# Optimization experiments

Hardware: AMD Instinct MI355X
Metric: run time of the kernel (lower is better)

The kernel has to match this reference:

```python
import jax, jax.numpy as jnp
import numpy as np

B, Lq, C, NH, NP, DFF = 8, 10000, 256, 8, 4, 1024
H_IMG, W_IMG = 100, 100
HD = C // NH


def _layer_norm(x, g, b, eps=1e-5):
    m = jnp.mean(x, -1, keepdims=True)
    v = jnp.mean((x - m) ** 2, -1, keepdims=True)
    return (x - m) / jnp.sqrt(v + eps) * g + b


def _bilinear_sample(value, loc, Hs, Ws):
    # value: [B, Lin, NH, HD]; loc: [B, Lq, NH, NP, 2] normalized to [0,1]
    vt = jnp.transpose(value, (0, 2, 1, 3))  # [B, NH, Lin, HD]
    # move to [B, NH, Lq, NP] layout once; grid_sample(align_corners=False) pixel coords
    x = jnp.transpose(loc[..., 0], (0, 2, 1, 3)) * Ws - 0.5
    y = jnp.transpose(loc[..., 1], (0, 2, 1, 3)) * Hs - 0.5
    x0 = jnp.floor(x); y0 = jnp.floor(y)
    lx = x - x0; ly = y - y0

    def corner(xi, yi, w):
        valid = (xi >= 0) & (xi < Ws) & (yi >= 0) & (yi < Hs)
        xc = jnp.clip(xi, 0, Ws - 1).astype(jnp.int32)
        yc = jnp.clip(yi, 0, Hs - 1).astype(jnp.int32)
        idx = (yc * Ws + xc).reshape(B, NH, Lq * NP, 1)
        v = jnp.take_along_axis(vt, idx, axis=2).reshape(B, NH, Lq, NP, HD)
        return v * (w * valid)[..., None]

    acc = corner(x0, y0, (1 - lx) * (1 - ly))
    acc = acc + corner(x0 + 1, y0, lx * (1 - ly))
    acc = acc + corner(x0, y0 + 1, (1 - lx) * ly)
    acc = acc + corner(x0 + 1, y0 + 1, lx * ly)
    return acc  # [B, NH, Lq, NP, HD]


def setup_inputs() -> dict:
    key = jax.random.key(0)
    ks = jax.random.split(key, 12)
    s = 0.02
    return {
        "query": jax.random.normal(ks[0], (B, Lq, C), jnp.float32),
        "src": jax.random.normal(ks[1], (B, H_IMG * W_IMG, C), jnp.float32),
        "reference_points": jax.random.uniform(ks[2], (B, Lq, 1, 2), jnp.float32),
        "spatial_shapes": jnp.array([[H_IMG, W_IMG]], dtype=jnp.int64),
        "level_start_index": jnp.array([0], dtype=jnp.int64),
        "W_off": jax.random.normal(ks[3], (C, NH * NP * 2), jnp.float32) * s,
        "b_off": jnp.zeros((NH * NP * 2,), jnp.float32),
        "W_aw": jax.random.normal(ks[4], (C, NH * NP), jnp.float32) * s,
        "b_aw": jnp.zeros((NH * NP,), jnp.float32),
        "W_val": jax.random.normal(ks[5], (C, C), jnp.float32) * s,
        "b_val": jnp.zeros((C,), jnp.float32),
        "W_out": jax.random.normal(ks[6], (C, C), jnp.float32) * s,
        "b_out": jnp.zeros((C,), jnp.float32),
        "g1": jnp.ones((C,), jnp.float32),
        "be1": jnp.zeros((C,), jnp.float32),
        "W1": jax.random.normal(ks[7], (C, DFF), jnp.float32) * s,
        "b1": jnp.zeros((DFF,), jnp.float32),
        "W2": jax.random.normal(ks[8], (DFF, C), jnp.float32) * s,
        "b2": jnp.zeros((C,), jnp.float32),
        "g2": jnp.ones((C,), jnp.float32),
        "be2": jnp.zeros((C,), jnp.float32),
    }


def reference(query, src, reference_points, spatial_shapes, level_start_index,
              W_off, b_off, W_aw, b_aw, W_val, b_val, W_out, b_out,
              g1, be1, W1, b1, W2, b2, g2, be2):
    Hs = spatial_shapes[0, 0]
    Ws = spatial_shapes[0, 1]
    # MSDeformAttn (n_levels = 1)
    value = (src @ W_val + b_val).reshape(B, -1, NH, HD)
    off = (query @ W_off + b_off).reshape(B, Lq, NH, NP, 2)
    aw = jax.nn.softmax((query @ W_aw + b_aw).reshape(B, Lq, NH, NP), axis=-1)
    normalizer = jnp.stack([Ws, Hs]).astype(query.dtype)  # (W, H)
    loc = reference_points[:, :, None] + off / normalizer  # [B,Lq,NH,NP,2]
    sampled = _bilinear_sample(value, loc, Hs, Ws)  # [B,NH,Lq,NP,HD]
    attn = jnp.einsum('bhqpd,bqhp->bqhd', sampled, aw).reshape(B, Lq, C)
    attn = attn @ W_out + b_out
    # residual + LN + FFN + LN
    q = _layer_norm(query + attn, g1, be1)
    ffn = jax.nn.relu(q @ W1 + b1) @ W2 + b2
    return _layer_norm(q + ffn, g2, be2)
```

## Files before the change

kernel.cpp:

```cpp
#include <hip/hip_runtime.h>
#include <hip/hip_bf16.h>

typedef __hip_bfloat16 bf16;
typedef unsigned short u16;
typedef short short8 __attribute__((ext_vector_type(8)));
typedef float f32x4 __attribute__((ext_vector_type(4)));

static constexpr int B_   = 8;
static constexpr int Lq_  = 10000;
static constexpr int C_   = 256;
static constexpr int NH_  = 8;
static constexpr int NP_  = 4;
static constexpr int HIMG = 100;
static constexpr int WIMG = 100;
static constexpr int LIN  = 10000;

__device__ __forceinline__ u16 f2bf(float x) {
    union { bf16 b; u16 u; } cv; cv.b = __float2bfloat16(x); return cv.u;
}
__device__ __forceinline__ float bf2f(u16 u) {
    return __uint_as_float((unsigned)u << 16);
}

__device__ __forceinline__ void gl_lds16(const void* g, void* l) {
    __builtin_amdgcn_global_load_lds(
        (const __attribute__((address_space(1))) void*)g,
        (__attribute__((address_space(3))) void*)l, 16, 0, 0);
}
__device__ __forceinline__ void drain_barrier() {
    asm volatile("s_waitcnt vmcnt(0) lgkmcnt(0)" ::: "memory");
    __builtin_amdgcn_s_barrier();
}

template <int AMODE, int EPI>
__global__ __launch_bounds__(512, 2) void gemm256(
    const void* __restrict__ Av, const u16* __restrict__ Bg,
    const float* __restrict__ bias, const void* __restrict__ resid,
    const float* __restrict__ gw, const float* __restrict__ bw,
    void* __restrict__ Cv, int K, int ldc)
{
    __shared__ __align__(16) u16 At[2][128 * 64];
    __shared__ __align__(16) u16 Bt[2][256 * 64];
    __shared__ float red[2][128][4];

    const int tid  = threadIdx.x;
    const int lane = tid & 63;
    const int w    = tid >> 6;
    const int wm   = w >> 2, wn = w & 3;
    const int m0   = blockIdx.x * 128;
    const int n0   = blockIdx.y * 256;
    const u16* BgB = Bg + (size_t)n0 * K;

    f32x4 acc[4][4];
#pragma unroll
    for (int i = 0; i < 4; ++i)
#pragma unroll
        for (int j = 0; j < 4; ++j) acc[i][j] = f32x4{0.f, 0.f, 0.f, 0.f};

    auto stageA = [&](int t) {
        const int kt = t << 6;
        if constexpr (AMODE == 0) {
            const int row = tid >> 2;
            const int k0  = (tid & 3) << 4;
            const float* s = (const float*)Av + (size_t)(m0 + row) * K + kt + k0;
            float4 v0 = *(const float4*)(s + 0);
            float4 v1 = *(const float4*)(s + 4);
            float4 v2 = *(const float4*)(s + 8);
            float4 v3 = *(const float4*)(s + 12);
            union { short8 s8; u16 u[8]; } ga, gb;
            ga.u[0]=f2bf(v0.x); ga.u[1]=f2bf(v0.y); ga.u[2]=f2bf(v0.z); ga.u[3]=f2bf(v0.w);
            ga.u[4]=f2bf(v1.x); ga.u[5]=f2bf(v1.y); ga.u[6]=f2bf(v1.z); ga.u[7]=f2bf(v1.w);
            gb.u[0]=f2bf(v2.x); gb.u[1]=f2bf(v2.y); gb.u[2]=f2bf(v2.z); gb.u[3]=f2bf(v2.w);
            gb.u[4]=f2bf(v3.x); gb.u[5]=f2bf(v3.y); gb.u[6]=f2bf(v3.z); gb.u[7]=f2bf(v3.w);
            u16* d = &At[t & 1][row * 64];
            *(short8*)&d[(k0)     ^ ((row & 7) << 3)] = ga.s8;
            *(short8*)&d[(k0 + 8) ^ ((row & 7) << 3)] = gb.s8;
        } else if constexpr (AMODE == 1) {
#pragma unroll
            for (int i = 0; i < 2; ++i) {
                const int rb  = w * 16 + i * 8;
                const int row = rb + (lane >> 3);
                const int gs  = (lane & 7) ^ (row & 7);
                gl_lds16((const u16*)Av + (size_t)(m0 + row) * K + kt + gs * 8,
                         &At[t & 1][rb * 64]);
            }
        } else {
#pragma unroll
            for (int i = 0; i < 2; ++i) {
                const int rb  = w * 16 + i * 8;
                const int row = rb + (lane >> 3);
                gl_lds16((const u16*)Av + (size_t)(m0 + row) * K + kt + (lane & 7) * 8,
                         &At[t & 1][rb * 64]);
            }
        }
    };
    auto stageB = [&](int t) {
        const int kt = t << 6;
#pragma unroll
        for (int i = 0; i < 4; ++i) {
            const int rb  = w * 32 + i * 8;
            const int row = rb + (lane >> 3);
            gl_lds16(BgB + (size_t)row * K + kt + (lane & 7) * 8,
                     &Bt[t & 1][rb * 64]);
        }
    };
    auto compute = [&](int t) {
        const u16* a = At[t & 1];
        const u16* b = Bt[t & 1];
#pragma unroll
        for (int ks = 0; ks < 2; ++ks) {
            const int ko = ks * 32 + ((lane >> 4) << 3);
            short8 bfr[4];
#pragma unroll
            for (int n = 0; n < 4; ++n) {
                const int nr = wn * 64 + n * 16 + (lane & 15);
                bfr[n] = *(const short8*)&b[nr * 64 + (ko ^ ((nr & 7) << 3))];
            }
#pragma unroll
            for (int m = 0; m < 4; ++m) {
                const int ar = wm * 64 + m * 16 + (lane & 15);
                const short8 af = *(const short8*)&a[ar * 64 + (ko ^ ((ar & 7) << 3))];
#pragma unroll
                for (int n = 0; n < 4; ++n)
                    acc[m][n] = __builtin_amdgcn_mfma_f32_16x16x32_bf16(
                        af, bfr[n], acc[m][n], 0, 0, 0);
            }
        }
    };

    stageA(0); stageB(0);
    drain_barrier();
    const int nt = K >> 6;
    for (int t = 0; t < nt; ++t) {
        if (t + 1 < nt) { stageA(t + 1); stageB(t + 1); }
        compute(t);
        drain_barrier();
    }

    float bcol[4], gcol[4], becol[4];
#pragma unroll
    for (int n = 0; n < 4; ++n) {
        const int col = wn * 64 + n * 16 + (lane & 15);
        bcol[n] = bias[n0 + col];
        if (EPI >= 2) { gcol[n] = gw[col]; becol[n] = bw[col]; }
    }

    if constexpr (EPI <= 1) {
        u16* Co = (u16*)Cv;
#pragma unroll
        for (int m = 0; m < 4; ++m)
#pragma unroll
            for (int r = 0; r < 4; ++r) {
                const int lr = wm * 64 + m * 16 + (lane >> 4) * 4 + r;
#pragma unroll
                for (int n = 0; n < 4; ++n) {
                    const int col = wn * 64 + n * 16 + (lane & 15);
                    float v = acc[m][n][r] + bcol[n];
                    if (EPI == 1) v = fmaxf(v, 0.f);
                    Co[(size_t)(m0 + lr) * ldc + n0 + col] = f2bf(v);
                }
            }
    } else {
        float s[4][4], s2[4][4];
#pragma unroll
        for (int m = 0; m < 4; ++m)
#pragma unroll
            for (int r = 0; r < 4; ++r) {
                const int lr = wm * 64 + m * 16 + (lane >> 4) * 4 + r;
                float ps = 0.f, ps2 = 0.f;
#pragma unroll
                for (int n = 0; n < 4; ++n) {
                    const int col = wn * 64 + n * 16 + (lane & 15);
                    float rv;
                    if constexpr (EPI == 2)
                        rv = ((const float*)resid)[(size_t)(m0 + lr) * 256 + col];
                    else
                        rv = bf2f(((const u16*)resid)[(size_t)(m0 + lr) * 256
                                                      + (col ^ ((lr & 7) << 3))]);
                    float v = acc[m][n][r] + bcol[n] + rv;
                    acc[m][n][r] = v;
                    ps += v; ps2 += v * v;
                }
#pragma unroll
                for (int o = 1; o < 16; o <<= 1) {
                    ps  += __shfl_xor(ps,  o);
                    ps2 += __shfl_xor(ps2, o);
                }
                s[m][r] = ps; s2[m][r] = ps2;
            }
        if ((lane & 15) == 0) {
#pragma unroll
            for (int m = 0; m < 4; ++m)
#pragma unroll
                for (int r = 0; r < 4; ++r) {
                    const int lr = wm * 64 + m * 16 + (lane >> 4) * 4 + r;
                    red[0][lr][wn] = s[m][r];
                    red[1][lr][wn] = s2[m][r];
                }
        }
        __syncthreads();
        if (tid < 128) {
            const float ss  = red[0][tid][0] + red[0][tid][1] + red[0][tid][2] + red[0][tid][3];
            const float ss2 = red[1][tid][0] + red[1][tid][1] + red[1][tid][2] + red[1][tid][3];
            const float mean = ss * (1.f / 256.f);
            const float var  = fmaxf(ss2 * (1.f / 256.f) - mean * mean, 0.f);
            red[0][tid][0] = mean;
            red[1][tid][0] = rsqrtf(var + 1e-5f);
        }
        __syncthreads();
#pragma unroll
        for (int m = 0; m < 4; ++m)
#pragma unroll
            for (int r = 0; r < 4; ++r) {
                const int lr = wm * 64 + m * 16 + (lane >> 4) * 4 + r;
                const float mean = red[0][lr][0];
                const float rstd = red[1][lr][0];
#pragma unroll
                for (int n = 0; n < 4; ++n) {
                    const int col = wn * 64 + n * 16 + (lane & 15);
                    const float o = (acc[m][n][r] - mean) * rstd * gcol[n] + becol[n];
                    if constexpr (EPI == 2)
                        ((u16*)Cv)[(size_t)(m0 + lr) * 256 + (col ^ ((lr & 7) << 3))] = f2bf(o);
                    else
                        ((float*)Cv)[(size_t)(m0 + lr) * 256 + col] = o;
                }
            }
    }
}

__global__ __launch_bounds__(256) void gemm_oaw(
    const float* __restrict__ Av, const u16* __restrict__ Bt,
    const float* __restrict__ bias, float* __restrict__ C,
    int M, int K, int Nreal, int ldc)
{
    __shared__ __align__(16) u16 Asl[2][128 * 32];
    __shared__ __align__(16) u16 Bsl[2][128 * 32];

    const int tid  = threadIdx.x;
    const int lane = tid & 63;
    const int w    = tid >> 6;
    const int wr   = (w >> 1) * 64;
    const int wc   = (w & 1) * 64;
    const int m0   = blockIdx.y * 128;
    const int n0   = blockIdx.x * 128;

    const int srow = lane >> 2;
    const int scol = (lane & 3) << 3;
    const u16* bG = Bt + (size_t)(n0 + w * 32 + srow) * K + scol;
    const size_t rstep16 = (size_t)16 * K;

    const int ar  = lane >> 3;
    const int ac  = (lane & 7) << 2;
    const float* aGf = Av + (size_t)(m0 + w * 32 + ar) * K + ac;

    const int aRoff = (wr + (lane & 15)) * 32 + (lane >> 4) * 8;
    const int bRoff = (wc + (lane & 15)) * 32 + (lane >> 4) * 8;

    f32x4 acc[4][4];
#pragma unroll
    for (int i = 0; i < 4; ++i)
#pragma unroll
        for (int j = 0; j < 4; ++j) acc[i][j] = f32x4{0.f, 0.f, 0.f, 0.f};

    float4 a4[4];
    const int nt = K >> 5;

#pragma unroll
    for (int rep = 0; rep < 4; ++rep)
        a4[rep] = *(const float4*)(aGf + (size_t)(rep * 8) * K);
#pragma unroll
    for (int rep = 0; rep < 4; ++rep) {
        ushort4 v{f2bf(a4[rep].x), f2bf(a4[rep].y), f2bf(a4[rep].z), f2bf(a4[rep].w)};
        *(ushort4*)&Asl[0][(w * 32 + rep * 8 + ar) * 32 + ac] = v;
    }
    gl_lds16(bG, &Bsl[0][(w * 32) * 32]);
    gl_lds16(bG + rstep16, &Bsl[0][(w * 32 + 16) * 32]);
    drain_barrier();

    for (int t = 0; t < nt; ++t) {
        const int cur = t & 1, nxt = cur ^ 1;
        const int k0n = (t + 1) << 5;
        const bool has_next = (t + 1 < nt);
        if (has_next) {
#pragma unroll
            for (int rep = 0; rep < 4; ++rep)
                a4[rep] = *(const float4*)(aGf + k0n + (size_t)(rep * 8) * K);
            gl_lds16(bG + k0n, &Bsl[nxt][(w * 32) * 32]);
            gl_lds16(bG + k0n + rstep16, &Bsl[nxt][(w * 32 + 16) * 32]);
        }
        short8 af[4], bfr[4];
#pragma unroll
        for (int m = 0; m < 4; ++m) af[m]  = *(const short8*)&Asl[cur][aRoff + m * 16 * 32];
#pragma unroll
        for (int n = 0; n < 4; ++n) bfr[n] = *(const short8*)&Bsl[cur][bRoff + n * 16 * 32];
#pragma unroll
        for (int m = 0; m < 4; ++m)
#pragma unroll
            for (int n = 0; n < 4; ++n)
                acc[m][n] = __builtin_amdgcn_mfma_f32_16x16x32_bf16(
                    af[m], bfr[n], acc[m][n], 0, 0, 0);
        if (has_next) {
#pragma unroll
            for (int rep = 0; rep < 4; ++rep) {
                ushort4 v{f2bf(a4[rep].x), f2bf(a4[rep].y), f2bf(a4[rep].z), f2bf(a4[rep].w)};
                *(ushort4*)&Asl[nxt][(w * 32 + rep * 8 + ar) * 32 + ac] = v;
            }
        }
        drain_barrier();
    }

#pragma unroll
    for (int n = 0; n < 4; ++n) {
        const int gc = n0 + wc + n * 16 + (lane & 15);
        if (gc >= Nreal) continue;
        const float bv = bias[gc];
        const int gr0 = m0 + wr + (lane >> 4) * 4;
#pragma unroll
        for (int m = 0; m < 4; ++m)
#pragma unroll
            for (int r = 0; r < 4; ++r)
                C[(size_t)(gr0 + m * 16 + r) * ldc + gc] = acc[m][n][r] + bv;
    }
}

__global__ __launch_bounds__(256) void prep_all(
    const float* __restrict__ Wv, const float* __restrict__ Wo,
    const float* __restrict__ W1, const float* __restrict__ W2,
    const float* __restrict__ Woff, const float* __restrict__ Waw,
    const float* __restrict__ boff, const float* __restrict__ baw,
    u16* __restrict__ Wvs, u16* __restrict__ Wos,
    u16* __restrict__ W1g, u16* __restrict__ W2g,
    u16* __restrict__ Woa, float* __restrict__ boa)
{
    const int idx = blockIdx.x * 256 + threadIdx.x;
    if (idx < 65536) {
        const int n = idx >> 8, kd = idx & 255;
        const int k = (kd & ~63) | ((kd & 63) ^ ((n & 7) << 3));
        Wvs[idx] = f2bf(Wv[(size_t)k * 256 + n]);
    } else if (idx < 131072) {
        const int i = idx - 65536, n = i >> 8, kd = i & 255;
        const int k = (kd & ~63) | ((kd & 63) ^ ((n & 7) << 3));
        Wos[i] = f2bf(Wo[(size_t)k * 256 + n]);
    } else if (idx < 393216) {
        const int i = idx - 131072, n = i >> 8, kd = i & 255;
        const int k = (kd & ~63) | ((kd & 63) ^ ((n & 7) << 3));
        W1g[i] = f2bf(W1[(size_t)k * 1024 + n]);
    } else if (idx < 655360) {
        const int i = idx - 393216, n = i >> 10, kd = i & 1023;
        const int k = (kd & ~63) | ((kd & 63) ^ ((n & 7) << 3));
        W2g[i] = f2bf(W2[(size_t)k * 256 + n]);
    } else if (idx < 688128) {
        const int i = idx - 655360, n = i >> 8, k = i & 255;
        float v = 0.f;
        if (n < 64)      v = Woff[(size_t)k * 64 + n];
        else if (n < 96) v = Waw[(size_t)k * 32 + (n - 64)];
        Woa[i] = f2bf(v);
    } else if (idx < 688256) {
        const int i = idx - 688128;
        boa[i] = (i < 64) ? boff[i] : (i < 96 ? baw[i - 64] : 0.f);
    }
}

__global__ __launch_bounds__(256) void sample_attn(
    const u16* __restrict__ val, const float* __restrict__ oaw,
    const float* __restrict__ refp, u16* __restrict__ attn)
{
    const int t   = threadIdx.x;
    const int gid = blockIdx.x * 64 + (t >> 2);
    const int c0  = (t & 3) << 3;
    const int h   = gid & (NH_ - 1);
    const int bq  = gid >> 3;

    const float* row = oaw + (size_t)bq * 96;
    const float rx = refp[(size_t)bq * 2 + 0] * (float)WIMG;
    const float ry = refp[(size_t)bq * 2 + 1] * (float)HIMG;

    const float4 aw4 = *(const float4*)(row + 64 + h * 4);
    const float mx = fmaxf(fmaxf(aw4.x, aw4.y), fmaxf(aw4.z, aw4.w));
    const float e0 = __expf(aw4.x - mx), e1 = __expf(aw4.y - mx);
    const float e2 = __expf(aw4.z - mx), e3 = __expf(aw4.w - mx);
    const float inv = 1.f / (e0 + e1 + e2 + e3);
    const float w4[4] = {e0 * inv, e1 * inv, e2 * inv, e3 * inv};

    const int b = bq / Lq_;
    const u16* vb = val + (size_t)b * LIN * C_ + h * 32 + c0;

    float acc[8] = {};
#pragma unroll
    for (int p = 0; p < NP_; ++p) {
        const float2 off = *(const float2*)(row + (h * 4 + p) * 2);
        const float x = rx + off.x - 0.5f;
        const float y = ry + off.y - 0.5f;
        const float xf = floorf(x), yf = floorf(y);
        const float lx = x - xf, ly = y - yf;
        const int x0 = (int)xf, y0 = (int)yf;
        const float wp = w4[p];
        const float w00 = wp * (1.f - lx) * (1.f - ly);
        const float w10 = wp * lx * (1.f - ly);
        const float w01 = wp * (1.f - lx) * ly;
        const float w11 = wp * lx * ly;

#pragma unroll
        for (int c = 0; c < 4; ++c) {
            const int xi = x0 + (c & 1);
            const int yi = y0 + (c >> 1);
            const float wc = (c == 0) ? w00 : (c == 1) ? w10 : (c == 2) ? w01 : w11;
            const bool v = ((unsigned)xi < (unsigned)WIMG) & ((unsigned)yi < (unsigned)HIMG);
            const int idx = v ? (yi * WIMG + xi) : 0;
            const float w = v ? wc : 0.f;
            const short8 d = *(const short8*)(vb + (size_t)idx * C_);
#pragma unroll
            for (int j = 0; j < 8; ++j)
                acc[j] = fmaf(w, bf2f(((const u16*)&d)[j]), acc[j]);
        }
    }

    union { short8 s; u16 u[8]; } o;
#pragma unroll
    for (int j = 0; j < 8; ++j) o.u[j] = f2bf(acc[j]);
    *(short8*)(attn + (size_t)bq * C_ + h * 32 + c0) = o.s;
}

extern "C" void kernel_launch(void* const* d_in, const int* in_sizes, int n_in,
                              void* d_out, int out_size, void* d_ws, size_t ws_size,
                              hipStream_t stream)
{
    const float* query = (const float*)d_in[0];
    const float* src   = (const float*)d_in[1];
    const float* refp  = (const float*)d_in[2];
    const float* W_off = (const float*)d_in[5];
    const float* b_off = (const float*)d_in[6];
    const float* W_aw  = (const float*)d_in[7];
    const float* b_aw  = (const float*)d_in[8];
    const float* W_val = (const float*)d_in[9];
    const float* b_val = (const float*)d_in[10];
    const float* W_out = (const float*)d_in[11];
    const float* b_out = (const float*)d_in[12];
    const float* g1    = (const float*)d_in[13];
    const float* be1   = (const float*)d_in[14];
    const float* W1    = (const float*)d_in[15];
    const float* b1    = (const float*)d_in[16];
    const float* W2    = (const float*)d_in[17];
    const float* b2    = (const float*)d_in[18];
    const float* g2    = (const float*)d_in[19];
    const float* be2   = (const float*)d_in[20];
    float* out = (float*)d_out;

    char* ws = (char*)d_ws;

    u16*  val  = (u16*)(ws + 0);
    float* oaw = (float*)(ws + 40960000);
    u16*  attn = (u16*)(ws + 71680000);
    u16*  q1b  = (u16*)(ws + 112640000);
    u16*  h    = (u16*)(ws + 153600000);
    u16*  Wvs  = (u16*)(ws + 317440000);
    u16*  Wos  = (u16*)(ws + 317440000 + 131072);
    u16*  W1g  = (u16*)(ws + 317440000 + 262144);
    u16*  W2g  = (u16*)(ws + 317440000 + 786432);
    u16*  Woa  = (u16*)(ws + 317440000 + 1310720);
    float* boa = (float*)(ws + 317440000 + 1376256);

    prep_all<<<2689, 256, 0, stream>>>(W_val, W_out, W1, W2, W_off, W_aw,
                                       b_off, b_aw, Wvs, Wos, W1g, W2g,
                                       Woa, boa);

    gemm256<0, 0><<<dim3(625, 1), 512, 0, stream>>>(
        src, Wvs, b_val, nullptr, nullptr, nullptr, val, 256, 256);

    gemm_oaw<<<dim3(1, 625), 256, 0, stream>>>(
        query, Woa, boa, oaw, B_ * Lq_, 256, 96, 96);

    sample_attn<<<10000, 256, 0, stream>>>(val, oaw, refp, attn);

    gemm256<1, 2><<<dim3(625, 1), 512, 0, stream>>>(
        attn, Wos, b_out, query, g1, be1, q1b, 256, 256);

    gemm256<2, 1><<<dim3(625, 4), 512, 0, stream>>>(
        q1b, W1g, b1, nullptr, nullptr, nullptr, h, 256, 1024);

    gemm256<1, 3><<<dim3(625, 1), 512, 0, stream>>>(
        h, W2g, b2, q1b, g2, be2, out, 1024, 256);
}
```

Baseline: 360.4 us.

## Fuse FFN up and down GEMMs into one kernel keeping hidden activations on-chip

Replaces the separate W1 GEMM (writing a bf16 hidden tensor to global memory) and the W2 GEMM with LayerNorm epilogue by a single ffn_wave kernel. Each wave holds its 16-row strip of q1 in registers and loops over 128-wide hidden chunks, staging pre-swizzled W1/W2 tiles into LDS with double buffering. ReLU'd hidden chunks go through a per-wave LDS scratch and are immediately multiplied by W2 into register accumulators. This removes the large h write/read round trip and one launch, at the cost of heavy register pressure (many accumulators plus A fragments) and re-streaming all weights per block.

```diff
diff --git a/kernel.cpp b/kernel.cpp
--- a/kernel.cpp
+++ b/kernel.cpp
@@ -32,12 +32,12 @@
     __builtin_amdgcn_s_barrier();
 }
 
-template <int AMODE, int EPI>
+template <bool AF32, bool LN>
 __global__ __launch_bounds__(512, 2) void gemm256(
     const void* __restrict__ Av, const u16* __restrict__ Bg,
-    const float* __restrict__ bias, const void* __restrict__ resid,
+    const float* __restrict__ bias, const float* __restrict__ resid,
     const float* __restrict__ gw, const float* __restrict__ bw,
-    void* __restrict__ Cv, int K, int ldc)
+    u16* __restrict__ Co, int K)
 {
     __shared__ __align__(16) u16 At[2][128 * 64];
     __shared__ __align__(16) u16 Bt[2][256 * 64];
@@ -48,8 +48,6 @@
     const int w    = tid >> 6;
     const int wm   = w >> 2, wn = w & 3;
     const int m0   = blockIdx.x * 128;
-    const int n0   = blockIdx.y * 256;
-    const u16* BgB = Bg + (size_t)n0 * K;
 
     f32x4 acc[4][4];
 #pragma unroll
@@ -59,7 +57,7 @@
 
     auto stageA = [&](int t) {
         const int kt = t << 6;
-        if constexpr (AMODE == 0) {
+        if constexpr (AF32) {
             const int row = tid >> 2;
             const int k0  = (tid & 3) << 4;
             const float* s = (const float*)Av + (size_t)(m0 + row) * K + kt + k0;
@@ -75,7 +73,7 @@
             u16* d = &At[t & 1][row * 64];
             *(short8*)&d[(k0)     ^ ((row & 7) << 3)] = ga.s8;
             *(short8*)&d[(k0 + 8) ^ ((row & 7) << 3)] = gb.s8;
-        } else if constexpr (AMODE == 1) {
+        } else {
 #pragma unroll
             for (int i = 0; i < 2; ++i) {
                 const int rb  = w * 16 + i * 8;
@@ -84,14 +82,6 @@
                 gl_lds16((const u16*)Av + (size_t)(m0 + row) * K + kt + gs * 8,
                          &At[t & 1][rb * 64]);
             }
-        } else {
-#pragma unroll
-            for (int i = 0; i < 2; ++i) {
-                const int rb  = w * 16 + i * 8;
-                const int row = rb + (lane >> 3);
-                gl_lds16((const u16*)Av + (size_t)(m0 + row) * K + kt + (lane & 7) * 8,
-                         &At[t & 1][rb * 64]);
-            }
         }
     };
     auto stageB = [&](int t) {
@@ -100,7 +90,7 @@
         for (int i = 0; i < 4; ++i) {
             const int rb  = w * 32 + i * 8;
             const int row = rb + (lane >> 3);
-            gl_lds16(BgB + (size_t)row * K + kt + (lane & 7) * 8,
+            gl_lds16(Bg + (size_t)row * K + kt + (lane & 7) * 8,
                      &Bt[t & 1][rb * 64]);
         }
     };
@@ -141,12 +131,11 @@
 #pragma unroll
     for (int n = 0; n < 4; ++n) {
         const int col = wn * 64 + n * 16 + (lane & 15);
-        bcol[n] = bias[n0 + col];
-        if (EPI >= 2) { gcol[n] = gw[col]; becol[n] = bw[col]; }
-    }
-
-    if constexpr (EPI <= 1) {
-        u16* Co = (u16*)Cv;
+        bcol[n] = bias[col];
+        if (LN) { gcol[n] = gw[col]; becol[n] = bw[col]; }
+    }
+
+    if constexpr (!LN) {
 #pragma unroll
         for (int m = 0; m < 4; ++m)
 #pragma unroll
@@ -155,9 +144,7 @@
 #pragma unroll
                 for (int n = 0; n < 4; ++n) {
                     const int col = wn * 64 + n * 16 + (lane & 15);
-                    float v = acc[m][n][r] + bcol[n];
-                    if (EPI == 1) v = fmaxf(v, 0.f);
-                    Co[(size_t)(m0 + lr) * ldc + n0 + col] = f2bf(v);
+                    Co[(size_t)(m0 + lr) * 256 + col] = f2bf(acc[m][n][r] + bcol[n]);
                 }
             }
     } else {
@@ -171,13 +158,8 @@
 #pragma unroll
                 for (int n = 0; n < 4; ++n) {
                     const int col = wn * 64 + n * 16 + (lane & 15);
-                    float rv;
-                    if constexpr (EPI == 2)
-                        rv = ((const float*)resid)[(size_t)(m0 + lr) * 256 + col];
-                    else
-                        rv = bf2f(((const u16*)resid)[(size_t)(m0 + lr) * 256
-                                                      + (col ^ ((lr & 7) << 3))]);
-                    float v = acc[m][n][r] + bcol[n] + rv;
+                    float v = acc[m][n][r] + bcol[n]
+                            + resid[(size_t)(m0 + lr) * 256 + col];
                     acc[m][n][r] = v;
                     ps += v; ps2 += v * v;
                 }
@@ -219,12 +201,153 @@
                 for (int n = 0; n < 4; ++n) {
                     const int col = wn * 64 + n * 16 + (lane & 15);
                     const float o = (acc[m][n][r] - mean) * rstd * gcol[n] + becol[n];
-                    if constexpr (EPI == 2)
-                        ((u16*)Cv)[(size_t)(m0 + lr) * 256 + (col ^ ((lr & 7) << 3))] = f2bf(o);
-                    else
-                        ((float*)Cv)[(size_t)(m0 + lr) * 256 + col] = o;
+                    Co[(size_t)(m0 + lr) * 256 + col] = f2bf(o);
                 }
             }
+    }
+}
+
+__global__ __launch_bounds__(512, 2) void ffn_wave(
+    const u16* __restrict__ q1l, const u16* __restrict__ W1L,
+    const u16* __restrict__ W2L, const float* __restrict__ b1,
+    const float* __restrict__ b2, const float* __restrict__ g2w,
+    const float* __restrict__ be2, float* __restrict__ out)
+{
+    __shared__ __align__(16) u16 R0[16384];
+    __shared__ __align__(16) u16 R1[16384];
+    __shared__ __align__(16) u16 Hsc[8][2048];
+
+    const int tid  = threadIdx.x;
+    const int lane = tid & 63;
+    const int w    = tid >> 6;
+    const int m0   = blockIdx.x * 128;
+    const int strip = w * 16;
+    const int l15  = lane & 15;
+    const int lq   = lane >> 4;
+
+    short8 af[8];
+    {
+        const u16* aG = q1l + (size_t)(m0 + strip + l15) * 256 + lq * 8;
+#pragma unroll
+        for (int t = 0; t < 8; ++t)
+            af[t] = *(const short8*)(aG + t * 32);
+    }
+
+    auto stage = [&](const u16* src, u16* dst) {
+#pragma unroll
+        for (int i = 0; i < 4; ++i)
+            gl_lds16(src + (w * 4 + i) * 512 + lane * 8,
+                     dst + (w * 4 + i) * 512);
+    };
+
+    f32x4 acc2[16];
+#pragma unroll
+    for (int i = 0; i < 16; ++i) acc2[i] = f32x4{0.f, 0.f, 0.f, 0.f};
+
+    f32x4 acc1[8];
+    auto g1half = [&](const u16* Rg, int half) {
+#pragma unroll
+        for (int tl = 0; tl < 4; ++tl) {
+            const int t = half * 4 + tl;
+#pragma unroll
+            for (int nf = 0; nf < 8; ++nf) {
+                const int n = nf * 16 + l15;
+                const short8 bfr = *(const short8*)
+                    &Rg[n * 128 + (((tl * 4 + lq) ^ (n & 7)) << 3)];
+                acc1[nf] = __builtin_amdgcn_mfma_f32_16x16x32_bf16(
+                    af[t], bfr, acc1[nf], 0, 0, 0);
+            }
+        }
+    };
+    auto g2half = [&](const u16* Rg, int hu) {
+#pragma unroll
+        for (int ul = 0; ul < 2; ++ul) {
+            const int u = hu * 2 + ul;
+            const short8 hf = *(const short8*)
+                &Hsc[w][l15 * 128 + (((u * 4 + lq) ^ (l15 & 7)) << 3)];
+#pragma unroll
+            for (int nf = 0; nf < 16; ++nf) {
+                const int n = nf * 16 + l15;
+                const short8 bfr = *(const short8*)
+                    &Rg[n * 64 + (((ul * 4 + lq) ^ (n & 7)) << 3)];
+                acc2[nf] = __builtin_amdgcn_mfma_f32_16x16x32_bf16(
+                    hf, bfr, acc2[nf], 0, 0, 0);
+            }
+        }
+    };
+
+    stage(W1L, R0);
+    drain_barrier();
+
+    for (int c = 0; c < 8; ++c) {
+        const u16* w1c = W1L + (size_t)c * 32768;
+        const u16* w2c = W2L + (size_t)c * 32768;
+#pragma unroll
+        for (int i = 0; i < 8; ++i) acc1[i] = f32x4{0.f, 0.f, 0.f, 0.f};
+
+        stage(w1c + 16384, R1);
+        g1half(R0, 0);
+        drain_barrier();
+        stage(w2c, R0);
+        g1half(R1, 1);
+        drain_barrier();
+
+        stage(w2c + 16384, R1);
+        {
+            float b1v[8];
+#pragma unroll
+            for (int nf = 0; nf < 8; ++nf)
+                b1v[nf] = b1[c * 128 + nf * 16 + l15];
+#pragma unroll
+            for (int nf = 0; nf < 8; ++nf) {
+                const int col = nf * 16 + l15;
+#pragma unroll
+                for (int r = 0; r < 4; ++r) {
+                    const int row = lq * 4 + r;
+                    Hsc[w][row * 128 + (((col >> 3) ^ (row & 7)) << 3) + (col & 7)]
+                        = f2bf(fmaxf(acc1[nf][r] + b1v[nf], 0.f));
+                }
+            }
+        }
+        g2half(R0, 0);
+        drain_barrier();
+        if (c < 7) stage(w1c + 32768, R0);
+        g2half(R1, 1);
+        drain_barrier();
+    }
+
+    float bcol[16], gcol[16], becol[16];
+#pragma unroll
+    for (int nf = 0; nf < 16; ++nf) {
+        const int col = nf * 16 + l15;
+        bcol[nf] = b2[col]; gcol[nf] = g2w[col]; becol[nf] = be2[col];
+    }
+#pragma unroll
+    for (int r = 0; r < 4; ++r) {
+        const int grow = m0 + strip + lq * 4 + r;
+        float ps = 0.f, ps2 = 0.f;
+        float v[16];
+#pragma unroll
+        for (int nf = 0; nf < 16; ++nf) {
+            const int col = nf * 16 + l15;
+            v[nf] = acc2[nf][r] + bcol[nf]
+                  + bf2f(q1l[(size_t)grow * 256 + col]);
+            ps += v[nf]; ps2 += v[nf] * v[nf];
+        }
+#pragma unroll
+        for (int o = 1; o < 16; o <<= 1) {
+            ps  += __shfl_xor(ps,  o);
+            ps2 += __shfl_xor(ps2, o);
+        }
+        const float mean = ps * (1.f / 256.f);
+        const float var  = fmaxf(ps2 * (1.f / 256.f) - mean * mean, 0.f);
+        const float rstd = rsqrtf(var + 1e-5f);
+#pragma unroll
+        for (int nf = 0; nf < 16; ++nf) {
+            const int col = nf * 16 + l15;
+            out[(size_t)grow * 256 + col] =
+                (v[nf] - mean) * rstd * gcol[nf] + becol[nf];
+        }
     }
 }
 
@@ -288,9 +411,9 @@
             gl_lds16(bG + k0n, &Bsl[nxt][(w * 32) * 32]);
             gl_lds16(bG + k0n + rstep16, &Bsl[nxt][(w * 32 + 16) * 32]);
         }
-        short8 af[4], bfr[4];
-#pragma unroll
-        for (int m = 0; m < 4; ++m) af[m]  = *(const short8*)&Asl[cur][aRoff + m * 16 * 32];
+        short8 afr[4], bfr[4];
+#pragma unroll
+        for (int m = 0; m < 4; ++m) afr[m] = *(const short8*)&Asl[cur][aRoff + m * 16 * 32];
 #pragma unroll
         for (int n = 0; n < 4; ++n) bfr[n] = *(const short8*)&Bsl[cur][bRoff + n * 16 * 32];
 #pragma unroll
@@ -298,7 +421,7 @@
 #pragma unroll
             for (int n = 0; n < 4; ++n)
                 acc[m][n] = __builtin_amdgcn_mfma_f32_16x16x32_bf16(
-                    af[m], bfr[n], acc[m][n], 0, 0, 0);
+                    afr[m], bfr[n], acc[m][n], 0, 0, 0);
         if (has_next) {
 #pragma unroll
             for (int rep = 0; rep < 4; ++rep) {
@@ -329,26 +452,34 @@
     const float* __restrict__ Woff, const float* __restrict__ Waw,
     const float* __restrict__ boff, const float* __restrict__ baw,
     u16* __restrict__ Wvs, u16* __restrict__ Wos,
-    u16* __restrict__ W1g, u16* __restrict__ W2g,
+    u16* __restrict__ W1L, u16* __restrict__ W2L,
     u16* __restrict__ Woa, float* __restrict__ boa)
 {
     const int idx = blockIdx.x * 256 + threadIdx.x;
     if (idx < 65536) {
         const int n = idx >> 8, kd = idx & 255;
-        const int k = (kd & ~63) | ((kd & 63) ^ ((n & 7) << 3));
-        Wvs[idx] = f2bf(Wv[(size_t)k * 256 + n]);
+        Wvs[idx] = f2bf(Wv[(size_t)(kd ^ ((n & 7) << 3)) * 256 + n]);
     } else if (idx < 131072) {
         const int i = idx - 65536, n = i >> 8, kd = i & 255;
-        const int k = (kd & ~63) | ((kd & 63) ^ ((n & 7) << 3));
-        Wos[i] = f2bf(Wo[(size_t)k * 256 + n]);
+        Wos[i] = f2bf(Wo[(size_t)(kd ^ ((n & 7) << 3)) * 256 + n]);
     } else if (idx < 393216) {
-        const int i = idx - 131072, n = i >> 8, kd = i & 255;
-        const int k = (kd & ~63) | ((kd & 63) ^ ((n & 7) << 3));
-        W1g[i] = f2bf(W1[(size_t)k * 1024 + n]);
+        const int i = idx - 131072;
+        const int c2 = i >> 14;
+        const int n  = (i >> 7) & 127;
+        const int kg = (i >> 3) & 15;
+        const int j  = i & 7;
+        const int c = c2 >> 1, half = c2 & 1;
+        const int k = half * 128 + ((kg ^ (n & 7)) << 3) + j;
+        W1L[i] = f2bf(W1[(size_t)k * 1024 + c * 128 + n]);
     } else if (idx < 655360) {
-        const int i = idx - 393216, n = i >> 10, kd = i & 1023;
-        const int k = (kd & ~63) | ((kd & 63) ^ ((n & 7) << 3));
-        W2g[i] = f2bf(W2[(size_t)k * 256 + n]);
+        const int i = idx - 393216;
+        const int c2 = i >> 14;
+        const int n  = (i >> 6) & 255;
+        const int kg = (i >> 3) & 7;
+        const int j  = i & 7;
+        const int c = c2 >> 1, half = c2 & 1;
+        const int k = c * 128 + half * 64 + ((kg ^ (n & 7)) << 3) + j;
+        W2L[i] = f2bf(W2[(size_t)k * 256 + n]);
     } else if (idx < 688128) {
         const int i = idx - 655360, n = i >> 8, k = i & 255;
         float v = 0.f;
@@ -447,37 +578,33 @@
     float* out = (float*)d_out;
 
     char* ws = (char*)d_ws;
+    const int R = B_ * Lq_;
 
     u16*  val  = (u16*)(ws + 0);
     float* oaw = (float*)(ws + 40960000);
     u16*  attn = (u16*)(ws + 71680000);
-    u16*  q1b  = (u16*)(ws + 112640000);
-    u16*  h    = (u16*)(ws + 153600000);
-    u16*  Wvs  = (u16*)(ws + 317440000);
-    u16*  Wos  = (u16*)(ws + 317440000 + 131072);
-    u16*  W1g  = (u16*)(ws + 317440000 + 262144);
-    u16*  W2g  = (u16*)(ws + 317440000 + 786432);
-    u16*  Woa  = (u16*)(ws + 317440000 + 1310720);
-    float* boa = (float*)(ws + 317440000 + 1376256);
+    u16*  q1l  = (u16*)(ws + 112640000);
+    u16*  Wvs  = (u16*)(ws + 153600000);
+    u16*  Wos  = (u16*)(ws + 153600000 + 131072);
+    u16*  W1L  = (u16*)(ws + 153600000 + 262144);
+    u16*  W2L  = (u16*)(ws + 153600000 + 786432);
+    u16*  Woa  = (u16*)(ws + 153600000 + 1310720);
+    float* boa = (float*)(ws + 153600000 + 1376256);
 
     prep_all<<<2689, 256, 0, stream>>>(W_val, W_out, W1, W2, W_off, W_aw,
-                                       b_off, b_aw, Wvs, Wos, W1g, W2g,
+                                       b_off, b_aw, Wvs, Wos, W1L, W2L,
                                        Woa, boa);
 
-    gemm256<0, 0><<<dim3(625, 1), 512, 0, stream>>>(
-        src, Wvs, b_val, nullptr, nullptr, nullptr, val, 256, 256);
+    gemm256<true, false><<<625, 512, 0, stream>>>(
+        src, Wvs, b_val, nullptr, nullptr, nullptr, val, 256);
 
     gemm_oaw<<<dim3(1, 625), 256, 0, stream>>>(
-        query, Woa, boa, oaw, B_ * Lq_, 256, 96, 96);
+        query, Woa, boa, oaw, R, 256, 96, 96);
 
     sample_attn<<<10000, 256, 0, stream>>>(val, oaw, refp, attn);
 
-    gemm256<1, 2><<<dim3(625, 1), 512, 0, stream>>>(
-        attn, Wos, b_out, query, g1, be1, q1b, 256, 256);
-
-    gemm256<2, 1><<<dim3(625, 4), 512, 0, stream>>>(
-        q1b, W1g, b1, nullptr, nullptr, nullptr, h, 256, 1024);
-
-    gemm256<1, 3><<<dim3(625, 1), 512, 0, stream>>>(
-        h, W2g, b2, q1b, g2, be2, out, 1024, 256);
-}
+    gemm256<false, true><<<625, 512, 0, stream>>>(
+        attn, Wos, b_out, query, g1, be1, q1l, 256);
+
+    ffn_wave<<<625, 512, 0, stream>>>(q1l, W1L, W2L, b1, b2, g2, be2, out);
+}
```

After: 322.1 us (median of 3 runs). -10.6%, faster.
